# Kernel optimization log

Hardware: AMD Instinct MI355X
Metric: run time of the kernel (lower is better)

The kernel has to match this reference:

```python
import jax, jax.numpy as jnp
import numpy as np

N_NODES = 100000


def setup_inputs() -> dict:
    key = jax.random.key(0)
    k1, k2, k3 = jax.random.split(key, 3)
    x = jax.random.normal(k1, (N_NODES, 64), dtype=jnp.float32)
    edge_index = jax.random.randint(k2, (2, 1250000), 0, N_NODES, dtype=jnp.int64)
    W = jax.random.normal(k3, (128, 64), dtype=jnp.float32) * (1.0 / np.sqrt(128.0))
    b = jnp.zeros((64,), dtype=jnp.float32)
    return {"x": x, "edge_index": edge_index, "W": W, "b": b}


def reference(x, edge_index, W, b):
    n = x.shape[0]
    row, col = edge_index[0], edge_index[1]
    # scatter-add neighbor features onto destination nodes
    neigh = jax.ops.segment_sum(x[row], col, num_segments=n)          # [n, d]
    count = jax.ops.segment_sum(jnp.ones_like(col, dtype=x.dtype), col, num_segments=n)
    count = jnp.where(count == 0, jnp.asarray(1.0, x.dtype), count)   # avoid div-by-zero
    neigh = neigh / count[:, None]                                    # mean aggregation
    x_aggr = jnp.concatenate([x, neigh], axis=-1)                     # [n, 2d]
    out = x_aggr @ W + b                                              # [n, out_dim]
    return jax.nn.relu(out)  # dropout=0.0 (eval) -> identity
```

## Files before the change

### kernel.cpp

```cpp
#include <hip/hip_runtime.h>

#define D 64
#define NPB 64
#define THREADS 512
#define CAP 64

typedef int v4i __attribute__((ext_vector_type(4)));

__device__ __forceinline__ unsigned short f2bf(float f) {
  unsigned u = __float_as_uint(f);
  return (unsigned short)((u + 0x7FFFu + ((u >> 16) & 1u)) >> 16);
}
__device__ __forceinline__ float bf2f(unsigned short h) {
  return __uint_as_float(((unsigned)h) << 16);
}

__global__ __launch_bounds__(256) void prep0_kernel(
    const float* __restrict__ x, ushort* __restrict__ xh,
    int* __restrict__ cnt, int n, int total4) {
  int t = blockIdx.x * blockDim.x + threadIdx.x;
  int nth = gridDim.x * blockDim.x;
  for (int i = t; i < n; i += nth) cnt[i] = 0;
  for (int i = t; i < total4; i += nth) {
    float4 v = ((const float4*)x)[i];
    ushort4 h;
    h.x = f2bf(v.x); h.y = f2bf(v.y); h.z = f2bf(v.z); h.w = f2bf(v.w);
    ((ushort4*)xh)[i] = h;
  }
}

__global__ __launch_bounds__(256) void fill_xcd_kernel(
    const int* __restrict__ ei, int* __restrict__ cnt,
    int* __restrict__ bucket, int e, int qpc) {
  const int myx = blockIdx.x & 7;
  const int chunk = blockIdx.x >> 3;
  const int quads = e >> 2;
  const v4i* row4 = (const v4i*)ei;
  const v4i* col4 = (const v4i*)(ei + e);
  int qend = chunk * qpc + qpc;
  if (qend > quads) qend = quads;
  for (int q = chunk * qpc + threadIdx.x; q < qend; q += 256) {
    v4i r = __builtin_nontemporal_load(&row4[q]);
    v4i c = __builtin_nontemporal_load(&col4[q]);
    if (((c.x >> 11) & 7) == myx) {
      int p = atomicAdd(&cnt[c.x], 1);
      if (p < CAP) bucket[(size_t)c.x * CAP + p] = r.x * D;
    }
    if (((c.y >> 11) & 7) == myx) {
      int p = atomicAdd(&cnt[c.y], 1);
      if (p < CAP) bucket[(size_t)c.y * CAP + p] = r.y * D;
    }
    if (((c.z >> 11) & 7) == myx) {
      int p = atomicAdd(&cnt[c.z], 1);
      if (p < CAP) bucket[(size_t)c.z * CAP + p] = r.z * D;
    }
    if (((c.w >> 11) & 7) == myx) {
      int p = atomicAdd(&cnt[c.w], 1);
      if (p < CAP) bucket[(size_t)c.w * CAP + p] = r.w * D;
    }
  }
}

__global__ __launch_bounds__(THREADS, 8) void fused_bf_kernel(
    const float* __restrict__ x, const ushort* __restrict__ xh,
    const int* __restrict__ cnt, const float* __restrict__ W,
    const float* __restrict__ b, float* __restrict__ out, int n) {
  __shared__ __align__(16) float xs[NPB * 128];

  const int lane = threadIdx.x & 63;
  const int wid  = threadIdx.x >> 6;
  const int base = blockIdx.x * NPB;
  const int* bucket = (const int*)out;
  const ushort* xpl = xh + lane;

  for (int m = 0; m < 8; ++m) {
    int nl = wid * 8 + m;
    int node = base + nl;
    if (node < n) {
      int dg = cnt[node];
      int dc = dg < CAP ? dg : CAP;
      int bk = bucket[(size_t)node * CAP + lane];
      float xown = x[(size_t)node * D + lane];
      float s0 = 0.f, s1 = 0.f, s2 = 0.f, s3 = 0.f;
      float s4 = 0.f, s5 = 0.f, s6 = 0.f, s7 = 0.f;
      int p = 0;
      for (; p + 8 <= dc; p += 8) {
        int a0 = __shfl(bk, p),     a1 = __shfl(bk, p + 1);
        int a2 = __shfl(bk, p + 2), a3 = __shfl(bk, p + 3);
        int a4 = __shfl(bk, p + 4), a5 = __shfl(bk, p + 5);
        int a6 = __shfl(bk, p + 6), a7 = __shfl(bk, p + 7);
        s0 += bf2f(xpl[a0]); s1 += bf2f(xpl[a1]);
        s2 += bf2f(xpl[a2]); s3 += bf2f(xpl[a3]);
        s4 += bf2f(xpl[a4]); s5 += bf2f(xpl[a5]);
        s6 += bf2f(xpl[a6]); s7 += bf2f(xpl[a7]);
      }
      for (; p + 4 <= dc; p += 4) {
        int a0 = __shfl(bk, p),     a1 = __shfl(bk, p + 1);
        int a2 = __shfl(bk, p + 2), a3 = __shfl(bk, p + 3);
        s0 += bf2f(xpl[a0]); s1 += bf2f(xpl[a1]);
        s2 += bf2f(xpl[a2]); s3 += bf2f(xpl[a3]);
      }
      for (; p < dc; ++p)
        s0 += bf2f(xpl[__shfl(bk, p)]);
      float sum = ((s0 + s1) + (s2 + s3)) + ((s4 + s5) + (s6 + s7));
      float inv = (dg > 0) ? (1.0f / (float)dg) : 0.0f;
      xs[nl * 128 + lane]      = xown;
      xs[nl * 128 + 64 + lane] = sum * inv;
    } else {
      xs[nl * 128 + lane]      = 0.0f;
      xs[nl * 128 + 64 + lane] = 0.0f;
    }
  }
  __syncthreads();

  const int col = lane;
  float bias = b[col];
  float acc[8];
#pragma unroll
  for (int m = 0; m < 8; ++m) acc[m] = bias;

  for (int k = 0; k < 128; k += 4) {
    float w0 = W[(k + 0) * 64 + col];
    float w1 = W[(k + 1) * 64 + col];
    float w2 = W[(k + 2) * 64 + col];
    float w3 = W[(k + 3) * 64 + col];
#pragma unroll
    for (int m = 0; m < 8; ++m) {
      int nl = wid + m * 8;
      float4 xv = *(const float4*)&xs[nl * 128 + k];
      acc[m] = fmaf(xv.x, w0, acc[m]);
      acc[m] = fmaf(xv.y, w1, acc[m]);
      acc[m] = fmaf(xv.z, w2, acc[m]);
      acc[m] = fmaf(xv.w, w3, acc[m]);
    }
  }

#pragma unroll
  for (int m = 0; m < 8; ++m) {
    int node = base + wid + m * 8;
    if (node < n)
      out[(size_t)node * D + col] = fmaxf(acc[m], 0.0f);
  }
}

__global__ __launch_bounds__(256) void fill_cap_kernel(
    const int* __restrict__ ei, int* __restrict__ cnt,
    int* __restrict__ bucket, int e) {
  int t = blockIdx.x * blockDim.x + threadIdx.x;
  if (t * 4 >= e) return;
  int4 r4 = ((const int4*)ei)[t];
  int4 c4 = ((const int4*)(ei + e))[t];
  int p0 = atomicAdd(&cnt[c4.x], 1);
  int p1 = atomicAdd(&cnt[c4.y], 1);
  int p2 = atomicAdd(&cnt[c4.z], 1);
  int p3 = atomicAdd(&cnt[c4.w], 1);
  if (p0 < CAP) bucket[(size_t)c4.x * CAP + p0] = r4.x;
  if (p1 < CAP) bucket[(size_t)c4.y * CAP + p1] = r4.y;
  if (p2 < CAP) bucket[(size_t)c4.z * CAP + p2] = r4.z;
  if (p3 < CAP) bucket[(size_t)c4.w * CAP + p3] = r4.w;
}

__global__ __launch_bounds__(THREADS, 8) void fused_cap_kernel(
    const float* __restrict__ x, const int* __restrict__ cnt,
    const float* __restrict__ W, const float* __restrict__ b,
    float* __restrict__ out, int n) {
  __shared__ __align__(16) float xs[NPB * 128];
  const int lane = threadIdx.x & 63;
  const int wid  = threadIdx.x >> 6;
  const int base = blockIdx.x * NPB;
  const int* bucket = (const int*)out;

  for (int m = 0; m < 8; ++m) {
    int nl = wid * 8 + m;
    int node = base + nl;
    if (node < n) {
      int dg = cnt[node];
      int dc = dg < CAP ? dg : CAP;
      int bk = bucket[(size_t)node * CAP + lane];
      float xown = x[(size_t)node * D + lane];
      float s0 = 0.f, s1 = 0.f, s2 = 0.f, s3 = 0.f;
      int p = 0;
      for (; p + 4 <= dc; p += 4) {
        int a0 = __shfl(bk, p),     a1 = __shfl(bk, p + 1);
        int a2 = __shfl(bk, p + 2), a3 = __shfl(bk, p + 3);
        s0 += x[(size_t)a0 * D + lane];
        s1 += x[(size_t)a1 * D + lane];
        s2 += x[(size_t)a2 * D + lane];
        s3 += x[(size_t)a3 * D + lane];
      }
      for (; p < dc; ++p)
        s0 += x[(size_t)__shfl(bk, p) * D + lane];
      float sum = (s0 + s1) + (s2 + s3);
      float inv = (dg > 0) ? (1.0f / (float)dg) : 0.0f;
      xs[nl * 128 + lane]      = xown;
      xs[nl * 128 + 64 + lane] = sum * inv;
    } else {
      xs[nl * 128 + lane]      = 0.0f;
      xs[nl * 128 + 64 + lane] = 0.0f;
    }
  }
  __syncthreads();

  const int col = lane;
  float bias = b[col];
  float acc[8];
#pragma unroll
  for (int m = 0; m < 8; ++m) acc[m] = bias;
  for (int k = 0; k < 128; k += 4) {
    float w0 = W[(k + 0) * 64 + col];
    float w1 = W[(k + 1) * 64 + col];
    float w2 = W[(k + 2) * 64 + col];
    float w3 = W[(k + 3) * 64 + col];
#pragma unroll
    for (int m = 0; m < 8; ++m) {
      int nl = wid + m * 8;
      float4 xv = *(const float4*)&xs[nl * 128 + k];
      acc[m] = fmaf(xv.x, w0, acc[m]);
      acc[m] = fmaf(xv.y, w1, acc[m]);
      acc[m] = fmaf(xv.z, w2, acc[m]);
      acc[m] = fmaf(xv.w, w3, acc[m]);
    }
  }
#pragma unroll
  for (int m = 0; m < 8; ++m) {
    int node = base + wid + m * 8;
    if (node < n)
      out[(size_t)node * D + col] = fmaxf(acc[m], 0.0f);
  }
}

extern "C" void kernel_launch(void* const* d_in, const int* in_sizes, int n_in,
                              void* d_out, int out_size, void* d_ws, size_t ws_size,
                              hipStream_t stream) {
  const float* x = (const float*)d_in[0];
  const int* ei = (const int*)d_in[1];
  const float* W = (const float*)d_in[2];
  const float* b = (const float*)d_in[3];
  float* out = (float*)d_out;

  int n = in_sizes[0] / D;
  int e = in_sizes[1] / 2;
  int nblocks = (n + NPB - 1) / NPB;

  size_t xh_bytes = (size_t)n * D * sizeof(ushort);
  size_t need = xh_bytes + (size_t)n * sizeof(int) + 256;

  if (ws_size >= need && (e & 3) == 0 && n <= (1 << 17)) {
    ushort* xh = (ushort*)d_ws;
    int* cnt = (int*)((char*)d_ws + ((xh_bytes + 255) & ~(size_t)255));

    int total4 = n * D / 4;
    prep0_kernel<<<2048, 256, 0, stream>>>(x, xh, cnt, n, total4);

    int quads = e >> 2;
    int qpc = (quads + 255) / 256;
    fill_xcd_kernel<<<256 * 8, 256, 0, stream>>>(ei, cnt, (int*)d_out, e, qpc);

    fused_bf_kernel<<<nblocks, THREADS, 0, stream>>>(x, xh, cnt, W, b, out, n);
  } else {
    int* cnt = (int*)d_ws;
    (void)hipMemsetAsync(cnt, 0, (size_t)n * sizeof(int), stream);
    int quads = e / 4;
    fill_cap_kernel<<<(quads + 255) / 256, 256, 0, stream>>>(ei, cnt, (int*)d_out, e);
    fused_cap_kernel<<<nblocks, THREADS, 0, stream>>>(x, cnt, W, b, out, n);
  }
}
```

Measured before the change: 209.1 us.

## Use hardware XCC id with work-stealing tickets in fill; vectorize bf16 gather

The fill kernel now reads the real XCC id from a hardware register and pulls edge chunks through per-XCC atomic ticket counters, so each die only handles destinations whose counters live in its own L2, rather than relying on blockIdx-to-XCD round-robin. The fused kernel now gathers neighbor rows as 4-bf16 uint2 loads, with four edges processed per wave through 16-lane subgroups that are reduced with cross-lane shuffles. It also reads the node's own features from the bf16 copy instead of fp32 x. The changes add ticket atomics and a dependence on the undocumented XCC mapping, and the own-feature read now carries bf16 rounding error.

New measurement: 240.7 us. 15.1% more time.

```diff
diff --git a/kernel.cpp b/kernel.cpp
--- a/kernel.cpp
+++ b/kernel.cpp
@@ -17,9 +17,10 @@
 
 __global__ __launch_bounds__(256) void prep0_kernel(
     const float* __restrict__ x, ushort* __restrict__ xh,
-    int* __restrict__ cnt, int n, int total4) {
+    int* __restrict__ cnt, int* __restrict__ ticket, int n, int total4) {
   int t = blockIdx.x * blockDim.x + threadIdx.x;
   int nth = gridDim.x * blockDim.x;
+  if (t < 128) ticket[t] = 0;
   for (int i = t; i < n; i += nth) cnt[i] = 0;
   for (int i = t; i < total4; i += nth) {
     float4 v = ((const float4*)x)[i];
@@ -29,49 +30,62 @@
   }
 }
 
-__global__ __launch_bounds__(256) void fill_xcd_kernel(
+__global__ __launch_bounds__(256) void fill_aff_kernel(
     const int* __restrict__ ei, int* __restrict__ cnt,
-    int* __restrict__ bucket, int e, int qpc) {
-  const int myx = blockIdx.x & 7;
-  const int chunk = blockIdx.x >> 3;
+    int* __restrict__ bucket, int* __restrict__ ticket,
+    int e, int nchunks, int qpc) {
+  unsigned xcc;
+  asm volatile("s_getreg_b32 %0, hwreg(HW_REG_XCC_ID)" : "=s"(xcc));
+  const int cls = (int)(xcc & 7u);
   const int quads = e >> 2;
   const v4i* row4 = (const v4i*)ei;
   const v4i* col4 = (const v4i*)(ei + e);
-  int qend = chunk * qpc + qpc;
-  if (qend > quads) qend = quads;
-  for (int q = chunk * qpc + threadIdx.x; q < qend; q += 256) {
-    v4i r = __builtin_nontemporal_load(&row4[q]);
-    v4i c = __builtin_nontemporal_load(&col4[q]);
-    if (((c.x >> 11) & 7) == myx) {
-      int p = atomicAdd(&cnt[c.x], 1);
-      if (p < CAP) bucket[(size_t)c.x * CAP + p] = r.x * D;
-    }
-    if (((c.y >> 11) & 7) == myx) {
-      int p = atomicAdd(&cnt[c.y], 1);
-      if (p < CAP) bucket[(size_t)c.y * CAP + p] = r.y * D;
-    }
-    if (((c.z >> 11) & 7) == myx) {
-      int p = atomicAdd(&cnt[c.z], 1);
-      if (p < CAP) bucket[(size_t)c.z * CAP + p] = r.z * D;
-    }
-    if (((c.w >> 11) & 7) == myx) {
-      int p = atomicAdd(&cnt[c.w], 1);
-      if (p < CAP) bucket[(size_t)c.w * CAP + p] = r.w * D;
-    }
-  }
-}
-
-__global__ __launch_bounds__(THREADS, 8) void fused_bf_kernel(
-    const float* __restrict__ x, const ushort* __restrict__ xh,
-    const int* __restrict__ cnt, const float* __restrict__ W,
-    const float* __restrict__ b, float* __restrict__ out, int n) {
+  __shared__ int sh_chunk;
+  for (;;) {
+    __syncthreads();
+    if (threadIdx.x == 0) sh_chunk = atomicAdd(&ticket[cls * 16], 1);
+    __syncthreads();
+    int chunk = sh_chunk;
+    if (chunk >= nchunks) break;
+    int q0 = chunk * qpc;
+    int qe = q0 + qpc;
+    if (qe > quads) qe = quads;
+    for (int q = q0 + threadIdx.x; q < qe; q += 256) {
+      v4i r = __builtin_nontemporal_load(&row4[q]);
+      v4i c = __builtin_nontemporal_load(&col4[q]);
+      if (((c.x >> 11) & 7) == cls) {
+        int p = atomicAdd(&cnt[c.x], 1);
+        if (p < CAP) bucket[(size_t)c.x * CAP + p] = r.x * D;
+      }
+      if (((c.y >> 11) & 7) == cls) {
+        int p = atomicAdd(&cnt[c.y], 1);
+        if (p < CAP) bucket[(size_t)c.y * CAP + p] = r.y * D;
+      }
+      if (((c.z >> 11) & 7) == cls) {
+        int p = atomicAdd(&cnt[c.z], 1);
+        if (p < CAP) bucket[(size_t)c.z * CAP + p] = r.z * D;
+      }
+      if (((c.w >> 11) & 7) == cls) {
+        int p = atomicAdd(&cnt[c.w], 1);
+        if (p < CAP) bucket[(size_t)c.w * CAP + p] = r.w * D;
+      }
+    }
+  }
+}
+
+__global__ __launch_bounds__(THREADS, 8) void fused_v3_kernel(
+    const ushort* __restrict__ xh, const int* __restrict__ cnt,
+    const float* __restrict__ W, const float* __restrict__ b,
+    float* __restrict__ out, int n) {
   __shared__ __align__(16) float xs[NPB * 128];
 
   const int lane = threadIdx.x & 63;
   const int wid  = threadIdx.x >> 6;
   const int base = blockIdx.x * NPB;
+  const int sub  = lane >> 4;
+  const int fq   = lane & 15;
   const int* bucket = (const int*)out;
-  const ushort* xpl = xh + lane;
+  const ushort* xq = xh + fq * 4;
 
   for (int m = 0; m < 8; ++m) {
     int nl = wid * 8 + m;
@@ -79,33 +93,61 @@
     if (node < n) {
       int dg = cnt[node];
       int dc = dg < CAP ? dg : CAP;
-      int bk = bucket[(size_t)node * CAP + lane];
-      float xown = x[(size_t)node * D + lane];
-      float s0 = 0.f, s1 = 0.f, s2 = 0.f, s3 = 0.f;
-      float s4 = 0.f, s5 = 0.f, s6 = 0.f, s7 = 0.f;
+      int bk = 0;
+      if (lane < dc) bk = bucket[(size_t)node * CAP + lane];
+      float xown = bf2f(xh[(size_t)node * D + lane]);
+      float4 s0 = {0.f, 0.f, 0.f, 0.f};
+      float4 s1 = {0.f, 0.f, 0.f, 0.f};
       int p = 0;
       for (; p + 8 <= dc; p += 8) {
-        int a0 = __shfl(bk, p),     a1 = __shfl(bk, p + 1);
-        int a2 = __shfl(bk, p + 2), a3 = __shfl(bk, p + 3);
-        int a4 = __shfl(bk, p + 4), a5 = __shfl(bk, p + 5);
-        int a6 = __shfl(bk, p + 6), a7 = __shfl(bk, p + 7);
-        s0 += bf2f(xpl[a0]); s1 += bf2f(xpl[a1]);
-        s2 += bf2f(xpl[a2]); s3 += bf2f(xpl[a3]);
-        s4 += bf2f(xpl[a4]); s5 += bf2f(xpl[a5]);
-        s6 += bf2f(xpl[a6]); s7 += bf2f(xpl[a7]);
-      }
-      for (; p + 4 <= dc; p += 4) {
-        int a0 = __shfl(bk, p),     a1 = __shfl(bk, p + 1);
-        int a2 = __shfl(bk, p + 2), a3 = __shfl(bk, p + 3);
-        s0 += bf2f(xpl[a0]); s1 += bf2f(xpl[a1]);
-        s2 += bf2f(xpl[a2]); s3 += bf2f(xpl[a3]);
-      }
-      for (; p < dc; ++p)
-        s0 += bf2f(xpl[__shfl(bk, p)]);
-      float sum = ((s0 + s1) + (s2 + s3)) + ((s4 + s5) + (s6 + s7));
+        int a0 = __shfl(bk, p + sub);
+        int a1 = __shfl(bk, p + 4 + sub);
+        uint2 h0 = *(const uint2*)(xq + a0);
+        uint2 h1 = *(const uint2*)(xq + a1);
+        s0.x += __uint_as_float(h0.x << 16);
+        s0.y += __uint_as_float(h0.x & 0xffff0000u);
+        s0.z += __uint_as_float(h0.y << 16);
+        s0.w += __uint_as_float(h0.y & 0xffff0000u);
+        s1.x += __uint_as_float(h1.x << 16);
+        s1.y += __uint_as_float(h1.x & 0xffff0000u);
+        s1.z += __uint_as_float(h1.y << 16);
+        s1.w += __uint_as_float(h1.y & 0xffff0000u);
+      }
+      if (p + 4 <= dc) {
+        int a0 = __shfl(bk, p + sub);
+        uint2 h0 = *(const uint2*)(xq + a0);
+        s0.x += __uint_as_float(h0.x << 16);
+        s0.y += __uint_as_float(h0.x & 0xffff0000u);
+        s0.z += __uint_as_float(h0.y << 16);
+        s0.w += __uint_as_float(h0.y & 0xffff0000u);
+        p += 4;
+      }
+      int rem = dc - p;
+      if (rem > 0) {
+        int idx = p + (sub < rem ? sub : 0);
+        int a = __shfl(bk, idx);
+        if (sub < rem) {
+          uint2 h = *(const uint2*)(xq + a);
+          s1.x += __uint_as_float(h.x << 16);
+          s1.y += __uint_as_float(h.x & 0xffff0000u);
+          s1.z += __uint_as_float(h.y << 16);
+          s1.w += __uint_as_float(h.y & 0xffff0000u);
+        }
+      }
+      float4 s;
+      s.x = s0.x + s1.x; s.y = s0.y + s1.y;
+      s.z = s0.z + s1.z; s.w = s0.w + s1.w;
+      s.x += __shfl_xor(s.x, 16); s.y += __shfl_xor(s.y, 16);
+      s.z += __shfl_xor(s.z, 16); s.w += __shfl_xor(s.w, 16);
+      s.x += __shfl_xor(s.x, 32); s.y += __shfl_xor(s.y, 32);
+      s.z += __shfl_xor(s.z, 32); s.w += __shfl_xor(s.w, 32);
       float inv = (dg > 0) ? (1.0f / (float)dg) : 0.0f;
-      xs[nl * 128 + lane]      = xown;
-      xs[nl * 128 + 64 + lane] = sum * inv;
+      xs[nl * 128 + lane] = xown;
+      if (sub == 0) {
+        float4 o;
+        o.x = s.x * inv; o.y = s.y * inv; o.z = s.z * inv; o.w = s.w * inv;
+        *(float4*)&xs[nl * 128 + 64 + fq * 4] = o;
+      }
     } else {
       xs[nl * 128 + lane]      = 0.0f;
       xs[nl * 128 + 64 + lane] = 0.0f;
@@ -243,20 +285,24 @@
   int nblocks = (n + NPB - 1) / NPB;
 
   size_t xh_bytes = (size_t)n * D * sizeof(ushort);
-  size_t need = xh_bytes + (size_t)n * sizeof(int) + 256;
+  size_t cnt_bytes = (size_t)n * sizeof(int);
+  size_t need = xh_bytes + 256 + cnt_bytes + 256 + 128 * sizeof(int);
 
   if (ws_size >= need && (e & 3) == 0 && n <= (1 << 17)) {
     ushort* xh = (ushort*)d_ws;
     int* cnt = (int*)((char*)d_ws + ((xh_bytes + 255) & ~(size_t)255));
+    int* ticket = (int*)((char*)cnt + ((cnt_bytes + 255) & ~(size_t)255));
 
     int total4 = n * D / 4;
-    prep0_kernel<<<2048, 256, 0, stream>>>(x, xh, cnt, n, total4);
+    prep0_kernel<<<2048, 256, 0, stream>>>(x, xh, cnt, ticket, n, total4);
 
     int quads = e >> 2;
-    int qpc = (quads + 255) / 256;
-    fill_xcd_kernel<<<256 * 8, 256, 0, stream>>>(ei, cnt, (int*)d_out, e, qpc);
-
-    fused_bf_kernel<<<nblocks, THREADS, 0, stream>>>(x, xh, cnt, W, b, out, n);
+    int nchunks = 2048;
+    int qpc = (quads + nchunks - 1) / nchunks;
+    fill_aff_kernel<<<2048, 256, 0, stream>>>(ei, cnt, (int*)d_out, ticket,
+                                              e, nchunks, qpc);
+
+    fused_v3_kernel<<<nblocks, THREADS, 0, stream>>>(xh, cnt, W, b, out, n);
   } else {
     int* cnt = (int*)d_ws;
     (void)hipMemsetAsync(cnt, 0, (size_t)n * sizeof(int), stream);
```

## Merge prep, bucket fill and aggregation into one cooperative persistent kernel

Applied to the files above, without the earlier changes.

Replaces the three separate launches (bf16 conversion and count reset, XCD-partitioned bucket fill, fused gather+GEMM) with a single cooperative kernel that uses grid.sync between phases. The final phase becomes persistent, looping over node groups. It also reads the self features from the bf16 copy instead of fp32 and loads bucket entries only for lanes below the degree. The goal is to remove launch gaps and tail effects between kernels. In exchange it pays for two grid-wide barriers, runs the fill phase with a different block count, and loses some precision on the self-feature half of the input.

Result: slower. 392.0 us (+87.5%).

```diff
diff --git a/kernel.cpp b/kernel.cpp
--- a/kernel.cpp
+++ b/kernel.cpp
@@ -1,8 +1,10 @@
 #include <hip/hip_runtime.h>
+#include <hip/hip_cooperative_groups.h>
+
+namespace cg = cooperative_groups;
 
 #define D 64
 #define NPB 64
-#define THREADS 512
 #define CAP 64
 
 typedef int v4i __attribute__((ext_vector_type(4)));
@@ -15,131 +17,135 @@
   return __uint_as_float(((unsigned)h) << 16);
 }
 
-__global__ __launch_bounds__(256) void prep0_kernel(
-    const float* __restrict__ x, ushort* __restrict__ xh,
-    int* __restrict__ cnt, int n, int total4) {
-  int t = blockIdx.x * blockDim.x + threadIdx.x;
-  int nth = gridDim.x * blockDim.x;
-  for (int i = t; i < n; i += nth) cnt[i] = 0;
-  for (int i = t; i < total4; i += nth) {
+__global__ __launch_bounds__(512) void mega_kernel(
+    const float* __restrict__ x, const int* __restrict__ ei,
+    const float* __restrict__ W, const float* __restrict__ bv,
+    ushort* __restrict__ xh, int* __restrict__ cnt,
+    float* __restrict__ out, int n, int e, int ngroups, int qpc) {
+  cg::grid_group grid = cg::this_grid();
+  __shared__ __align__(16) float xs[NPB * 128];
+
+  const int tid = blockIdx.x * 512 + threadIdx.x;
+  const int nth = gridDim.x * 512;
+  const int lane = threadIdx.x & 63;
+  const int wid  = threadIdx.x >> 6;
+
+  for (int i = tid; i < n; i += nth) cnt[i] = 0;
+  const int total4 = n * D / 4;
+  for (int i = tid; i < total4; i += nth) {
     float4 v = ((const float4*)x)[i];
     ushort4 h;
     h.x = f2bf(v.x); h.y = f2bf(v.y); h.z = f2bf(v.z); h.w = f2bf(v.w);
     ((ushort4*)xh)[i] = h;
   }
-}
-
-__global__ __launch_bounds__(256) void fill_xcd_kernel(
-    const int* __restrict__ ei, int* __restrict__ cnt,
-    int* __restrict__ bucket, int e, int qpc) {
-  const int myx = blockIdx.x & 7;
-  const int chunk = blockIdx.x >> 3;
-  const int quads = e >> 2;
-  const v4i* row4 = (const v4i*)ei;
-  const v4i* col4 = (const v4i*)(ei + e);
-  int qend = chunk * qpc + qpc;
-  if (qend > quads) qend = quads;
-  for (int q = chunk * qpc + threadIdx.x; q < qend; q += 256) {
-    v4i r = __builtin_nontemporal_load(&row4[q]);
-    v4i c = __builtin_nontemporal_load(&col4[q]);
-    if (((c.x >> 11) & 7) == myx) {
-      int p = atomicAdd(&cnt[c.x], 1);
-      if (p < CAP) bucket[(size_t)c.x * CAP + p] = r.x * D;
-    }
-    if (((c.y >> 11) & 7) == myx) {
-      int p = atomicAdd(&cnt[c.y], 1);
-      if (p < CAP) bucket[(size_t)c.y * CAP + p] = r.y * D;
-    }
-    if (((c.z >> 11) & 7) == myx) {
-      int p = atomicAdd(&cnt[c.z], 1);
-      if (p < CAP) bucket[(size_t)c.z * CAP + p] = r.z * D;
-    }
-    if (((c.w >> 11) & 7) == myx) {
-      int p = atomicAdd(&cnt[c.w], 1);
-      if (p < CAP) bucket[(size_t)c.w * CAP + p] = r.w * D;
-    }
-  }
-}
-
-__global__ __launch_bounds__(THREADS, 8) void fused_bf_kernel(
-    const float* __restrict__ x, const ushort* __restrict__ xh,
-    const int* __restrict__ cnt, const float* __restrict__ W,
-    const float* __restrict__ b, float* __restrict__ out, int n) {
-  __shared__ __align__(16) float xs[NPB * 128];
-
-  const int lane = threadIdx.x & 63;
-  const int wid  = threadIdx.x >> 6;
-  const int base = blockIdx.x * NPB;
+  grid.sync();
+
+  {
+    const int cls = blockIdx.x & 7;
+    const int chunk = blockIdx.x >> 3;
+    const int quads = e >> 2;
+    const v4i* row4 = (const v4i*)ei;
+    const v4i* col4 = (const v4i*)(ei + e);
+    int* bucket = (int*)out;
+    int q0 = chunk * qpc;
+    int qe = q0 + qpc;
+    if (qe > quads) qe = quads;
+    for (int q = q0 + threadIdx.x; q < qe; q += 512) {
+      v4i r = __builtin_nontemporal_load(&row4[q]);
+      v4i c = __builtin_nontemporal_load(&col4[q]);
+      if (((c.x >> 11) & 7) == cls) {
+        int p = atomicAdd(&cnt[c.x], 1);
+        if (p < CAP) bucket[(size_t)c.x * CAP + p] = r.x * D;
+      }
+      if (((c.y >> 11) & 7) == cls) {
+        int p = atomicAdd(&cnt[c.y], 1);
+        if (p < CAP) bucket[(size_t)c.y * CAP + p] = r.y * D;
+      }
+      if (((c.z >> 11) & 7) == cls) {
+        int p = atomicAdd(&cnt[c.z], 1);
+        if (p < CAP) bucket[(size_t)c.z * CAP + p] = r.z * D;
+      }
+      if (((c.w >> 11) & 7) == cls) {
+        int p = atomicAdd(&cnt[c.w], 1);
+        if (p < CAP) bucket[(size_t)c.w * CAP + p] = r.w * D;
+      }
+    }
+  }
+  grid.sync();
+
   const int* bucket = (const int*)out;
   const ushort* xpl = xh + lane;
-
-  for (int m = 0; m < 8; ++m) {
-    int nl = wid * 8 + m;
-    int node = base + nl;
-    if (node < n) {
-      int dg = cnt[node];
-      int dc = dg < CAP ? dg : CAP;
-      int bk = bucket[(size_t)node * CAP + lane];
-      float xown = x[(size_t)node * D + lane];
-      float s0 = 0.f, s1 = 0.f, s2 = 0.f, s3 = 0.f;
-      float s4 = 0.f, s5 = 0.f, s6 = 0.f, s7 = 0.f;
-      int p = 0;
-      for (; p + 8 <= dc; p += 8) {
-        int a0 = __shfl(bk, p),     a1 = __shfl(bk, p + 1);
-        int a2 = __shfl(bk, p + 2), a3 = __shfl(bk, p + 3);
-        int a4 = __shfl(bk, p + 4), a5 = __shfl(bk, p + 5);
-        int a6 = __shfl(bk, p + 6), a7 = __shfl(bk, p + 7);
-        s0 += bf2f(xpl[a0]); s1 += bf2f(xpl[a1]);
-        s2 += bf2f(xpl[a2]); s3 += bf2f(xpl[a3]);
-        s4 += bf2f(xpl[a4]); s5 += bf2f(xpl[a5]);
-        s6 += bf2f(xpl[a6]); s7 += bf2f(xpl[a7]);
-      }
-      for (; p + 4 <= dc; p += 4) {
-        int a0 = __shfl(bk, p),     a1 = __shfl(bk, p + 1);
-        int a2 = __shfl(bk, p + 2), a3 = __shfl(bk, p + 3);
-        s0 += bf2f(xpl[a0]); s1 += bf2f(xpl[a1]);
-        s2 += bf2f(xpl[a2]); s3 += bf2f(xpl[a3]);
-      }
-      for (; p < dc; ++p)
-        s0 += bf2f(xpl[__shfl(bk, p)]);
-      float sum = ((s0 + s1) + (s2 + s3)) + ((s4 + s5) + (s6 + s7));
-      float inv = (dg > 0) ? (1.0f / (float)dg) : 0.0f;
-      xs[nl * 128 + lane]      = xown;
-      xs[nl * 128 + 64 + lane] = sum * inv;
-    } else {
-      xs[nl * 128 + lane]      = 0.0f;
-      xs[nl * 128 + 64 + lane] = 0.0f;
-    }
-  }
-  __syncthreads();
-
-  const int col = lane;
-  float bias = b[col];
-  float acc[8];
-#pragma unroll
-  for (int m = 0; m < 8; ++m) acc[m] = bias;
-
-  for (int k = 0; k < 128; k += 4) {
-    float w0 = W[(k + 0) * 64 + col];
-    float w1 = W[(k + 1) * 64 + col];
-    float w2 = W[(k + 2) * 64 + col];
-    float w3 = W[(k + 3) * 64 + col];
-#pragma unroll
+  for (int g = blockIdx.x; g < ngroups; g += gridDim.x) {
+    const int base = g * NPB;
     for (int m = 0; m < 8; ++m) {
-      int nl = wid + m * 8;
-      float4 xv = *(const float4*)&xs[nl * 128 + k];
-      acc[m] = fmaf(xv.x, w0, acc[m]);
-      acc[m] = fmaf(xv.y, w1, acc[m]);
-      acc[m] = fmaf(xv.z, w2, acc[m]);
-      acc[m] = fmaf(xv.w, w3, acc[m]);
-    }
-  }
-
-#pragma unroll
-  for (int m = 0; m < 8; ++m) {
-    int node = base + wid + m * 8;
-    if (node < n)
-      out[(size_t)node * D + col] = fmaxf(acc[m], 0.0f);
+      int nl = wid * 8 + m;
+      int node = base + nl;
+      if (node < n) {
+        int dg = cnt[node];
+        int dc = dg < CAP ? dg : CAP;
+        int bk = 0;
+        if (lane < dc) bk = bucket[(size_t)node * CAP + lane];
+        float xown = bf2f(xh[(size_t)node * D + lane]);
+        float s0 = 0.f, s1 = 0.f, s2 = 0.f, s3 = 0.f;
+        float s4 = 0.f, s5 = 0.f, s6 = 0.f, s7 = 0.f;
+        int p = 0;
+        for (; p + 8 <= dc; p += 8) {
+          int a0 = __shfl(bk, p),     a1 = __shfl(bk, p + 1);
+          int a2 = __shfl(bk, p + 2), a3 = __shfl(bk, p + 3);
+          int a4 = __shfl(bk, p + 4), a5 = __shfl(bk, p + 5);
+          int a6 = __shfl(bk, p + 6), a7 = __shfl(bk, p + 7);
+          s0 += bf2f(xpl[a0]); s1 += bf2f(xpl[a1]);
+          s2 += bf2f(xpl[a2]); s3 += bf2f(xpl[a3]);
+          s4 += bf2f(xpl[a4]); s5 += bf2f(xpl[a5]);
+          s6 += bf2f(xpl[a6]); s7 += bf2f(xpl[a7]);
+        }
+        for (; p + 4 <= dc; p += 4) {
+          int a0 = __shfl(bk, p),     a1 = __shfl(bk, p + 1);
+          int a2 = __shfl(bk, p + 2), a3 = __shfl(bk, p + 3);
+          s0 += bf2f(xpl[a0]); s1 += bf2f(xpl[a1]);
+          s2 += bf2f(xpl[a2]); s3 += bf2f(xpl[a3]);
+        }
+        for (; p < dc; ++p)
+          s0 += bf2f(xpl[__shfl(bk, p)]);
+        float sum = ((s0 + s1) + (s2 + s3)) + ((s4 + s5) + (s6 + s7));
+        float inv = (dg > 0) ? (1.0f / (float)dg) : 0.0f;
+        xs[nl * 128 + lane]      = xown;
+        xs[nl * 128 + 64 + lane] = sum * inv;
+      } else {
+        xs[nl * 128 + lane]      = 0.0f;
+        xs[nl * 128 + 64 + lane] = 0.0f;
+      }
+    }
+    __syncthreads();
+
+    const int col = lane;
+    float acc[8];
+#pragma unroll
+    for (int m = 0; m < 8; ++m) acc[m] = bv[col];
+
+    for (int k = 0; k < 128; k += 4) {
+      float w0 = W[(k + 0) * 64 + col];
+      float w1 = W[(k + 1) * 64 + col];
+      float w2 = W[(k + 2) * 64 + col];
+      float w3 = W[(k + 3) * 64 + col];
+#pragma unroll
+      for (int m = 0; m < 8; ++m) {
+        int nl = wid + m * 8;
+        float4 xv = *(const float4*)&xs[nl * 128 + k];
+        acc[m] = fmaf(xv.x, w0, acc[m]);
+        acc[m] = fmaf(xv.y, w1, acc[m]);
+        acc[m] = fmaf(xv.z, w2, acc[m]);
+        acc[m] = fmaf(xv.w, w3, acc[m]);
+      }
+    }
+
+#pragma unroll
+    for (int m = 0; m < 8; ++m) {
+      int node = base + wid + m * 8;
+      if (node < n)
+        out[(size_t)node * D + col] = fmaxf(acc[m], 0.0f);
+    }
+    __syncthreads();
   }
 }
 
@@ -147,20 +153,13 @@
     const int* __restrict__ ei, int* __restrict__ cnt,
     int* __restrict__ bucket, int e) {
   int t = blockIdx.x * blockDim.x + threadIdx.x;
-  if (t * 4 >= e) return;
-  int4 r4 = ((const int4*)ei)[t];
-  int4 c4 = ((const int4*)(ei + e))[t];
-  int p0 = atomicAdd(&cnt[c4.x], 1);
-  int p1 = atomicAdd(&cnt[c4.y], 1);
-  int p2 = atomicAdd(&cnt[c4.z], 1);
-  int p3 = atomicAdd(&cnt[c4.w], 1);
-  if (p0 < CAP) bucket[(size_t)c4.x * CAP + p0] = r4.x;
-  if (p1 < CAP) bucket[(size_t)c4.y * CAP + p1] = r4.y;
-  if (p2 < CAP) bucket[(size_t)c4.z * CAP + p2] = r4.z;
-  if (p3 < CAP) bucket[(size_t)c4.w * CAP + p3] = r4.w;
-}
-
-__global__ __launch_bounds__(THREADS, 8) void fused_cap_kernel(
+  if (t >= e) return;
+  int r = ei[t], c = ei[e + t];
+  int p = atomicAdd(&cnt[c], 1);
+  if (p < CAP) bucket[(size_t)c * CAP + p] = r;
+}
+
+__global__ __launch_bounds__(512) void fused_cap_kernel(
     const float* __restrict__ x, const int* __restrict__ cnt,
     const float* __restrict__ W, const float* __restrict__ b,
     float* __restrict__ out, int n) {
@@ -202,10 +201,9 @@
   __syncthreads();
 
   const int col = lane;
-  float bias = b[col];
   float acc[8];
 #pragma unroll
-  for (int m = 0; m < 8; ++m) acc[m] = bias;
+  for (int m = 0; m < 8; ++m) acc[m] = b[col];
   for (int k = 0; k < 128; k += 4) {
     float w0 = W[(k + 0) * 64 + col];
     float w1 = W[(k + 1) * 64 + col];
@@ -240,28 +238,34 @@
 
   int n = in_sizes[0] / D;
   int e = in_sizes[1] / 2;
-  int nblocks = (n + NPB - 1) / NPB;
+  int ngroups = (n + NPB - 1) / NPB;
 
   size_t xh_bytes = (size_t)n * D * sizeof(ushort);
-  size_t need = xh_bytes + (size_t)n * sizeof(int) + 256;
-
-  if (ws_size >= need && (e & 3) == 0 && n <= (1 << 17)) {
+  size_t need = xh_bytes + 256 + (size_t)n * sizeof(int);
+
+  int occ = 0, ncu = 256;
+  hipOccupancyMaxActiveBlocksPerMultiprocessor(&occ, mega_kernel, 512, 0);
+  hipDeviceGetAttribute(&ncu, hipDeviceAttributeMultiprocessorCount, 0);
+  int grid = occ * ncu;
+  grid &= ~7;
+
+  if (ws_size >= need && (e & 3) == 0 && n <= (1 << 17) && grid >= 8) {
     ushort* xh = (ushort*)d_ws;
     int* cnt = (int*)((char*)d_ws + ((xh_bytes + 255) & ~(size_t)255));
 
-    int total4 = n * D / 4;
-    prep0_kernel<<<2048, 256, 0, stream>>>(x, xh, cnt, n, total4);
-
     int quads = e >> 2;
-    int qpc = (quads + 255) / 256;
-    fill_xcd_kernel<<<256 * 8, 256, 0, stream>>>(ei, cnt, (int*)d_out, e, qpc);
-
-    fused_bf_kernel<<<nblocks, THREADS, 0, stream>>>(x, xh, cnt, W, b, out, n);
+    int nchunks = grid >> 3;
+    int qpc = (quads + nchunks - 1) / nchunks;
+
+    void* args[] = {(void*)&x, (void*)&ei, (void*)&W, (void*)&b,
+                    (void*)&xh, (void*)&cnt, (void*)&out,
+                    (void*)&n, (void*)&e, (void*)&ngroups, (void*)&qpc};
+    hipLaunchCooperativeKernel((void*)mega_kernel, dim3(grid), dim3(512),
+                               args, 0, stream);
   } else {
     int* cnt = (int*)d_ws;
     (void)hipMemsetAsync(cnt, 0, (size_t)n * sizeof(int), stream);
-    int quads = e / 4;
-    fill_cap_kernel<<<(quads + 255) / 256, 256, 0, stream>>>(ei, cnt, (int*)d_out, e);
-    fused_cap_kernel<<<nblocks, THREADS, 0, stream>>>(x, cnt, W, b, out, n);
-  }
-}
+    fill_cap_kernel<<<(e + 255) / 256, 256, 0, stream>>>(ei, cnt, (int*)d_out, e);
+    fused_cap_kernel<<<ngroups, 512, 0, stream>>>(x, cnt, W, b, out, n);
+  }
+}
```

## Merge bf16 conversion into fill kernel, memset counts, read self features as bf16

Applied to the files above, without the earlier changes.

The fp32-to-bf16 conversion of x now runs in dedicated blocks of the bucket-fill launch instead of a separate prep kernel, so the conversion and the edge scatter overlap. The count array is zeroed with a memset. The fused kernel reads each node's own features from the bf16 copy instead of fp32 x, and loads bucket entries only for lanes below the degree. This cuts one launch and some memory traffic, but the self features lose precision and the fill blocks now share the GPU with the conversion blocks.

New measurement: 210.3 us. About the same (+0.6%).

```diff
diff --git a/kernel.cpp b/kernel.cpp
--- a/kernel.cpp
+++ b/kernel.cpp
@@ -4,6 +4,7 @@
 #define NPB 64
 #define THREADS 512
 #define CAP 64
+#define CVTB 512
 
 typedef int v4i __attribute__((ext_vector_type(4)));
 
@@ -15,31 +16,30 @@
   return __uint_as_float(((unsigned)h) << 16);
 }
 
-__global__ __launch_bounds__(256) void prep0_kernel(
-    const float* __restrict__ x, ushort* __restrict__ xh,
-    int* __restrict__ cnt, int n, int total4) {
-  int t = blockIdx.x * blockDim.x + threadIdx.x;
-  int nth = gridDim.x * blockDim.x;
-  for (int i = t; i < n; i += nth) cnt[i] = 0;
-  for (int i = t; i < total4; i += nth) {
-    float4 v = ((const float4*)x)[i];
-    ushort4 h;
-    h.x = f2bf(v.x); h.y = f2bf(v.y); h.z = f2bf(v.z); h.w = f2bf(v.w);
-    ((ushort4*)xh)[i] = h;
-  }
-}
-
-__global__ __launch_bounds__(256) void fill_xcd_kernel(
-    const int* __restrict__ ei, int* __restrict__ cnt,
-    int* __restrict__ bucket, int e, int qpc) {
-  const int myx = blockIdx.x & 7;
-  const int chunk = blockIdx.x >> 3;
+__global__ __launch_bounds__(256) void fill_cvt_kernel(
+    const float* __restrict__ x, const int* __restrict__ ei,
+    ushort* __restrict__ xh, int* __restrict__ cnt,
+    int* __restrict__ bucket, int n, int e, int qpc) {
+  if (blockIdx.x < CVTB) {
+    const int total4 = n * D / 4;
+    for (int i = blockIdx.x * 256 + threadIdx.x; i < total4; i += CVTB * 256) {
+      float4 v = ((const float4*)x)[i];
+      ushort4 h;
+      h.x = f2bf(v.x); h.y = f2bf(v.y); h.z = f2bf(v.z); h.w = f2bf(v.w);
+      ((ushort4*)xh)[i] = h;
+    }
+    return;
+  }
+  const int fb = blockIdx.x - CVTB;
+  const int myx = fb & 7;
+  const int chunk = fb >> 3;
   const int quads = e >> 2;
   const v4i* row4 = (const v4i*)ei;
   const v4i* col4 = (const v4i*)(ei + e);
-  int qend = chunk * qpc + qpc;
-  if (qend > quads) qend = quads;
-  for (int q = chunk * qpc + threadIdx.x; q < qend; q += 256) {
+  int q0 = chunk * qpc;
+  int qe = q0 + qpc;
+  if (qe > quads) qe = quads;
+  for (int q = q0 + threadIdx.x; q < qe; q += 256) {
     v4i r = __builtin_nontemporal_load(&row4[q]);
     v4i c = __builtin_nontemporal_load(&col4[q]);
     if (((c.x >> 11) & 7) == myx) {
@@ -62,9 +62,9 @@
 }
 
 __global__ __launch_bounds__(THREADS, 8) void fused_bf_kernel(
-    const float* __restrict__ x, const ushort* __restrict__ xh,
-    const int* __restrict__ cnt, const float* __restrict__ W,
-    const float* __restrict__ b, float* __restrict__ out, int n) {
+    const ushort* __restrict__ xh, const int* __restrict__ cnt,
+    const float* __restrict__ W, const float* __restrict__ b,
+    float* __restrict__ out, int n) {
   __shared__ __align__(16) float xs[NPB * 128];
 
   const int lane = threadIdx.x & 63;
@@ -79,8 +79,9 @@
     if (node < n) {
       int dg = cnt[node];
       int dc = dg < CAP ? dg : CAP;
-      int bk = bucket[(size_t)node * CAP + lane];
-      float xown = x[(size_t)node * D + lane];
+      int bk = 0;
+      if (lane < dc) bk = bucket[(size_t)node * CAP + lane];
+      float xown = bf2f(xh[(size_t)node * D + lane]);
       float s0 = 0.f, s1 = 0.f, s2 = 0.f, s3 = 0.f;
       float s4 = 0.f, s5 = 0.f, s6 = 0.f, s7 = 0.f;
       int p = 0;
@@ -249,14 +250,14 @@
     ushort* xh = (ushort*)d_ws;
     int* cnt = (int*)((char*)d_ws + ((xh_bytes + 255) & ~(size_t)255));
 
-    int total4 = n * D / 4;
-    prep0_kernel<<<2048, 256, 0, stream>>>(x, xh, cnt, n, total4);
+    (void)hipMemsetAsync(cnt, 0, (size_t)n * sizeof(int), stream);
 
     int quads = e >> 2;
     int qpc = (quads + 255) / 256;
-    fill_xcd_kernel<<<256 * 8, 256, 0, stream>>>(ei, cnt, (int*)d_out, e, qpc);
-
-    fused_bf_kernel<<<nblocks, THREADS, 0, stream>>>(x, xh, cnt, W, b, out, n);
+    fill_cvt_kernel<<<CVTB + 256 * 8, 256, 0, stream>>>(
+        x, ei, xh, cnt, (int*)d_out, n, e, qpc);
+
+    fused_bf_kernel<<<nblocks, THREADS, 0, stream>>>(xh, cnt, W, b, out, n);
   } else {
     int* cnt = (int*)d_ws;
     (void)hipMemsetAsync(cnt, 0, (size_t)n * sizeof(int), stream);
```
